# Optimization experiments

Hardware: AMD Instinct MI355X
Metric: run time of the kernel (lower is better)

## Reference

```python
import jax, jax.numpy as jnp
import numpy as np

C = 16            # NCA_channels
LCD = 3           # living_channel_dim
ALPHA = 0.1       # alpha_living_threshold


def _alive(x):
    # F.max_pool3d(x[:, LCD], k=3, s=1, p=1) -> shape [B, D, H, W]
    a = x[:, LCD]
    return jax.lax.reduce_window(a, -jnp.inf, jax.lax.max,
                                 (1, 3, 3, 3), (1, 1, 1, 1), 'SAME')


def _thresh(alive):
    th = ALPHA * jnp.max(alive)
    return jnp.where(jnp.isnan(th), -jnp.inf, th)


def _pw(h, w, b):
    # 1x1x1 Conv3d == per-voxel matmul. h: [B,c,D,H,W], w: [o,c]
    return jnp.einsum('bcdhw,oc->bodhw', h, w) + b[None, :, None, None, None]


def _update(x, w_perc, b_perc, w1, b1, w2, b2, w3, b3):
    alive0 = _alive(x)
    pre_mask = alive0 > _thresh(alive0)
    # depthwise perception conv: C -> 3C, groups=C, k=3, pad=1
    out = jax.lax.conv_general_dilated(
        x, w_perc, (1, 1, 1), 'SAME',
        dimension_numbers=('NCDHW', 'OIDHW', 'NCDHW'),
        feature_group_count=C) + b_perc[None, :, None, None, None]
    # per-voxel MLP: 3C -> h -> h -> C (tanh on hidden layers only)
    out = jnp.tanh(_pw(out, w1, b1))
    out = jnp.tanh(_pw(out, w2, b2))
    out = _pw(out, w3, b3)
    # normalise=False, replace=False -> residual add
    x = x + out
    alive1 = _alive(x)
    post_mask = alive1 > _thresh(alive1)
    life = pre_mask & post_mask          # [B, D, H, W]
    # torch x * life_mask (broadcast valid for B=1)
    return x * life[:, None].astype(x.dtype)


def setup_inputs() -> dict:
    key = jax.random.key(0)
    ks = jax.random.split(key, 10)
    D = 96
    x = jax.random.normal(ks[0], (1, C, D, D, D), dtype=jnp.float32)
    s = 0.1  # keep tanh-NCA dynamics stable
    return {
        'x': x,
        'w_perc': jax.random.normal(ks[1], (3 * C, 1, 3, 3, 3), jnp.float32) * s,
        'b_perc': jax.random.normal(ks[2], (3 * C,), jnp.float32) * s,
        'w1': jax.random.normal(ks[3], (64, 3 * C), jnp.float32) * s,
        'b1': jax.random.normal(ks[4], (64,), jnp.float32) * s,
        'w2': jax.random.normal(ks[5], (64, 64), jnp.float32) * s,
        'b2': jax.random.normal(ks[6], (64,), jnp.float32) * s,
        'w3': jax.random.normal(ks[7], (C, 64), jnp.float32) * s,
        'b3': jax.random.normal(ks[8], (C,), jnp.float32) * s,
        'steps': 4,
        'reading_channel': 4,
        'policy_layers': 2,
        'inOut_out': 48,
    }


def reference(x, w_perc, b_perc, w1, b1, w2, b2, w3, b3,
              steps, reading_channel, policy_layers, inOut_out):
    del reading_channel, policy_layers  # only used for visualization/PCA paths
    for _ in range(steps):
        x = _update(x, w_perc, b_perc, w1, b1, w2, b2, w3, b3)
        # x[:, :, -1, inOutdim[1]:, :] = 0.0
        x = x.at[:, :, -1, inOut_out:, :].set(0.0)
    return x
```

## Files before the change

### kernel.cpp

```cpp
#include <hip/hip_runtime.h>

#define Cn 16
#define Dn 96
#define Sn (Dn*Dn*Dn)
#define DSTRIDE (Dn*Dn)
#define ENC_NEG_INF 0x007FFFFFu
#define PSTR 52

typedef float v2f __attribute__((ext_vector_type(2)));
typedef float v4f __attribute__((ext_vector_type(4)));
typedef _Float16 v4h __attribute__((ext_vector_type(4)));

__device__ __forceinline__ v2f ld2(const float* p){
    v2f r; __builtin_memcpy(&r, p, 8); return r;
}
__device__ __forceinline__ unsigned encf(float f){
    unsigned u = __float_as_uint(f);
    return (u & 0x80000000u) ? ~u : (u | 0x80000000u);
}
__device__ __forceinline__ float decf(unsigned u){
    return (u & 0x80000000u) ? __uint_as_float(u ^ 0x80000000u) : __uint_as_float(~u);
}
__device__ __forceinline__ float ftanh(float x){
    float t = __expf(2.0f*x);
    return 1.0f - __fdividef(2.0f, t + 1.0f);
}
__device__ __forceinline__ int clampi(int v){ return v<0?0:(v>Dn-1?Dn-1:v); }

__global__ void init_kernel(unsigned* __restrict__ maxv){
    if (threadIdx.x < 16) maxv[threadIdx.x] = ENC_NEG_INF;
}

__global__ void tr_kernel(const float* __restrict__ wp, const float* __restrict__ bp,
                          float* __restrict__ wpT, float* __restrict__ bpP){
    const int i = blockIdx.x*256 + threadIdx.x;
    if (i < 1296){ const int t=i/48, r=i%48, q=r>>4, c=r&15; wpT[i] = wp[(3*c+q)*27 + t]; }
    if (i < 48)  { const int q=i>>4, c=i&15; bpP[i] = bp[3*c + q]; }
}

__global__ void pack_kernel(const float* __restrict__ w1, const float* __restrict__ w2,
                            const float* __restrict__ w3,
                            _Float16* __restrict__ w1Ah, _Float16* __restrict__ w1Al,
                            _Float16* __restrict__ w2Ah, _Float16* __restrict__ w2Al,
                            _Float16* __restrict__ w3Ah, _Float16* __restrict__ w3Al){
    const int i = blockIdx.x*256 + threadIdx.x;
    const int e = i & 3, l = (i>>2) & 63, tile = i >> 8;
    const int lr = l & 15, lg = l >> 4;
    if (i < 3072){
        const int ks = tile % 3, mt = tile / 3;
        const int c = 4*lg + e;
        const float v = w1[(16*mt + lr)*48 + 3*c + ks];
        const _Float16 hh = (_Float16)v;
        w1Ah[i] = hh; w1Al[i] = (_Float16)(v - (float)hh);
    }
    if (i < 4096){
        const int ks = tile & 3, mt = tile >> 2;
        const float v = w2[(16*mt + lr)*64 + 16*ks + 4*lg + e];
        const _Float16 hh = (_Float16)v;
        w2Ah[i] = hh; w2Al[i] = (_Float16)(v - (float)hh);
    }
    if (i < 1024){
        const int ks = tile;
        const float v = w3[lr*64 + 16*ks + 4*lg + e];
        const _Float16 hh = (_Float16)v;
        w3Ah[i] = hh; w3Al[i] = (_Float16)(v - (float)hh);
    }
}

__global__ __launch_bounds__(256) void prep_kernel(const float* __restrict__ x3,
    unsigned char* __restrict__ maskA, unsigned* __restrict__ slot)
{
    const int idx = blockIdx.x*256 + threadIdx.x;
    maskA[idx] = 1;
    float v = x3[idx];
    #pragma unroll
    for (int o=32;o;o>>=1) v = fmaxf(v, __shfl_down(v, o));
    __shared__ float red[4];
    const int lane = threadIdx.x & 63, wid = threadIdx.x >> 6;
    if (lane==0) red[wid]=v;
    __syncthreads();
    if (threadIdx.x==0){
        float m = fmaxf(fmaxf(red[0],red[1]), fmaxf(red[2],red[3]));
        atomicMax(slot, encf(m));
    }
}

struct XBuf { float x[16]; float m; int v; };

__device__ __forceinline__ void prefetch_t(int t, int d, int h, int w,
    const float* __restrict__ xin, const unsigned char* __restrict__ min_, XBuf& B)
{
    const int zz = d + t/9 - 1;
    const int yy = h + (t/3)%3 - 1;
    const int xx = w + t%3 - 1;
    const int zc = clampi(zz), yc = clampi(yy), xc = clampi(xx);
    B.v = (zz==zc) & (yy==yc) & (xx==xc);
    const int noff = zc*DSTRIDE + yc*Dn + xc;
    B.m = (float)min_[noff];
    #pragma unroll
    for (int c=0;c<16;++c) B.x[c] = xin[(size_t)c*Sn + noff];
}

__device__ __forceinline__ void accum_t(int t, const XBuf& A,
    const float* __restrict__ wpT, v2f* pv)
{
    const float mv = A.v ? A.m : 0.0f;
    const v2f mvv = {mv, mv};
    const float* wrow = wpT + t*48;
    #pragma unroll
    for (int i=0;i<8;++i){
        v2f xv = {A.x[2*i], A.x[2*i+1]};
        v2f xm = xv * mvv;
        pv[i]    = __builtin_elementwise_fma(ld2(wrow + 2*i),      xm, pv[i]);
        pv[8+i]  = __builtin_elementwise_fma(ld2(wrow + 16 + 2*i), xm, pv[8+i]);
        pv[16+i] = __builtin_elementwise_fma(ld2(wrow + 32 + 2*i), xm, pv[16+i]);
    }
}

__global__ __launch_bounds__(256, 2) void update_kernel(
    const float* __restrict__ xin, const unsigned char* __restrict__ min_,
    float* __restrict__ xout,
    const float* __restrict__ wpT, const float* __restrict__ bpP,
    const _Float16* __restrict__ w1Ah, const _Float16* __restrict__ w1Al,
    const float* __restrict__ b1,
    const _Float16* __restrict__ w2Ah, const _Float16* __restrict__ w2Al,
    const float* __restrict__ b2,
    const _Float16* __restrict__ w3Ah, const _Float16* __restrict__ w3Al,
    const float* __restrict__ b3,
    unsigned* __restrict__ slot_post)
{
    __shared__ __align__(16) float sP[256*PSTR];

    const int tid = threadIdx.x;
    const int w = blockIdx.x*32 + (tid & 31);
    const int h = blockIdx.y*8  + (tid >> 5);
    const int d = blockIdx.z;
    const int idx = d*DSTRIDE + h*Dn + w;

    const int lane = tid & 63;
    const int wv   = tid >> 6;
    const int lr   = lane & 15;
    const int lg   = lane >> 4;

    v2f pv[24];
    #pragma unroll
    for (int j=0;j<24;++j) pv[j] = ld2(bpP + 2*j);

    XBuf A, B;
    prefetch_t(0, d, h, w, xin, min_, A);
    #pragma unroll 1
    for (int t=0; t<26; t+=2){
        prefetch_t(t+1, d, h, w, xin, min_, B);
        accum_t(t, A, wpT, pv);
        prefetch_t(t+2, d, h, w, xin, min_, A);
        accum_t(t+1, B, wpT, pv);
    }
    accum_t(26, A, wpT, pv);

    {
        float* pr = sP + tid*PSTR;
        #pragma unroll
        for (int jj=0;jj<12;++jj){
            v4f t = {pv[2*jj].x, pv[2*jj].y, pv[2*jj+1].x, pv[2*jj+1].y};
            __builtin_memcpy(pr + 4*jj, &t, 16);
        }
    }

    const int rowbase = 64*wv;
    #pragma unroll 1
    for (int half=0; half<2; ++half){
        const int r0 = rowbase + 32*half + lr;
        const int r1 = r0 + 16;

        __builtin_amdgcn_s_setprio(1);
        v4f c1[4][2];
        #pragma unroll
        for (int mt=0;mt<4;++mt){
            v4f bb; __builtin_memcpy(&bb, b1 + 16*mt + 4*lg, 16);
            c1[mt][0]=bb; c1[mt][1]=bb;
        }
        #pragma unroll
        for (int ks=0;ks<3;++ks){
            v4h bh[2], bl[2];
            #pragma unroll
            for (int jj=0;jj<2;++jj){
                v4f P;
                __builtin_memcpy(&P, sP + (jj ? r1 : r0)*PSTR + 16*ks + 4*lg, 16);
                v4h hi = {(_Float16)P[0],(_Float16)P[1],(_Float16)P[2],(_Float16)P[3]};
                v4h lo = {(_Float16)(P[0]-(float)hi[0]), (_Float16)(P[1]-(float)hi[1]),
                          (_Float16)(P[2]-(float)hi[2]), (_Float16)(P[3]-(float)hi[3])};
                bh[jj]=hi; bl[jj]=lo;
            }
            #pragma unroll
            for (int mt=0;mt<4;++mt){
                v4h ah, al;
                __builtin_memcpy(&ah, w1Ah + ((mt*3+ks)*64 + lane)*4, 8);
                __builtin_memcpy(&al, w1Al + ((mt*3+ks)*64 + lane)*4, 8);
                #pragma unroll
                for (int jj=0;jj<2;++jj){
                    c1[mt][jj] = __builtin_amdgcn_mfma_f32_16x16x16f16(ah, bh[jj], c1[mt][jj],0,0,0);
                    c1[mt][jj] = __builtin_amdgcn_mfma_f32_16x16x16f16(al, bh[jj], c1[mt][jj],0,0,0);
                    c1[mt][jj] = __builtin_amdgcn_mfma_f32_16x16x16f16(ah, bl[jj], c1[mt][jj],0,0,0);
                }
            }
        }

        v4f c2[4][2];
        #pragma unroll
        for (int mt=0;mt<4;++mt){
            v4f bb; __builtin_memcpy(&bb, b2 + 16*mt + 4*lg, 16);
            c2[mt][0]=bb; c2[mt][1]=bb;
        }
        #pragma unroll
        for (int ks=0;ks<4;++ks){
            v4h bh[2], bl[2];
            #pragma unroll
            for (int jj=0;jj<2;++jj){
                float t0=ftanh(c1[ks][jj][0]), t1=ftanh(c1[ks][jj][1]);
                float t2=ftanh(c1[ks][jj][2]), t3=ftanh(c1[ks][jj][3]);
                v4h hi = {(_Float16)t0,(_Float16)t1,(_Float16)t2,(_Float16)t3};
                v4h lo = {(_Float16)(t0-(float)hi[0]), (_Float16)(t1-(float)hi[1]),
                          (_Float16)(t2-(float)hi[2]), (_Float16)(t3-(float)hi[3])};
                bh[jj]=hi; bl[jj]=lo;
            }
            #pragma unroll
            for (int mt=0;mt<4;++mt){
                v4h ah, al;
                __builtin_memcpy(&ah, w2Ah + ((mt*4+ks)*64 + lane)*4, 8);
                __builtin_memcpy(&al, w2Al + ((mt*4+ks)*64 + lane)*4, 8);
                #pragma unroll
                for (int jj=0;jj<2;++jj){
                    c2[mt][jj] = __builtin_amdgcn_mfma_f32_16x16x16f16(ah, bh[jj], c2[mt][jj],0,0,0);
                    c2[mt][jj] = __builtin_amdgcn_mfma_f32_16x16x16f16(al, bh[jj], c2[mt][jj],0,0,0);
                    c2[mt][jj] = __builtin_amdgcn_mfma_f32_16x16x16f16(ah, bl[jj], c2[mt][jj],0,0,0);
                }
            }
        }

        v4f c3[2];
        {
            v4f bb; __builtin_memcpy(&bb, b3 + 4*lg, 16);
            c3[0]=bb; c3[1]=bb;
        }
        #pragma unroll
        for (int ks=0;ks<4;++ks){
            v4h bh[2], bl[2];
            #pragma unroll
            for (int jj=0;jj<2;++jj){
                float t0=ftanh(c2[ks][jj][0]), t1=ftanh(c2[ks][jj][1]);
                float t2=ftanh(c2[ks][jj][2]), t3=ftanh(c2[ks][jj][3]);
                v4h hi = {(_Float16)t0,(_Float16)t1,(_Float16)t2,(_Float16)t3};
                v4h lo = {(_Float16)(t0-(float)hi[0]), (_Float16)(t1-(float)hi[1]),
                          (_Float16)(t2-(float)hi[2]), (_Float16)(t3-(float)hi[3])};
                bh[jj]=hi; bl[jj]=lo;
            }
            v4h ah, al;
            __builtin_memcpy(&ah, w3Ah + (ks*64 + lane)*4, 8);
            __builtin_memcpy(&al, w3Al + (ks*64 + lane)*4, 8);
            #pragma unroll
            for (int jj=0;jj<2;++jj){
                c3[jj] = __builtin_amdgcn_mfma_f32_16x16x16f16(ah, bh[jj], c3[jj],0,0,0);
                c3[jj] = __builtin_amdgcn_mfma_f32_16x16x16f16(al, bh[jj], c3[jj],0,0,0);
                c3[jj] = __builtin_amdgcn_mfma_f32_16x16x16f16(ah, bl[jj], c3[jj],0,0,0);
            }
        }
        __builtin_amdgcn_s_setprio(0);

        __builtin_memcpy(sP + r0*PSTR + 4*lg, &c3[0], 16);
        __builtin_memcpy(sP + r1*PSTR + 4*lg, &c3[1], 16);
    }

    const float mcen = (float)min_[idx];
    const float* orow = sP + tid*PSTR;
    float v3 = 0.0f;
    #pragma unroll
    for (int c=0;c<16;++c){
        const float xn = fmaf(xin[(size_t)c*Sn+idx], mcen, orow[c]);
        xout[(size_t)c*Sn+idx] = xn;
        if (c==3) v3 = xn;
    }

    #pragma unroll
    for (int o=32;o;o>>=1) v3 = fmaxf(v3, __shfl_down(v3, o));
    if ((tid & 63) == 0) atomicMax(slot_post, encf(v3));
}

__global__ __launch_bounds__(256) void mask_kernel(
    const float* __restrict__ x3old, const unsigned char* __restrict__ min_,
    const float* __restrict__ x3new, unsigned char* __restrict__ mout,
    const unsigned* __restrict__ slot_pre, const unsigned* __restrict__ slot_post,
    unsigned* __restrict__ slot_next)
{
    const int idx = blockIdx.x*256 + threadIdx.x;
    const int w = idx % Dn;
    const int h = (idx / Dn) % Dn;
    const int d = idx / DSTRIDE;
    const float th0 = 0.1f * decf(*slot_pre);
    const float th1 = 0.1f * decf(*slot_post);
    float a0 = -INFINITY, a1 = -INFINITY;
    #pragma unroll
    for (int t=0;t<27;++t){
        const int dz=t/9-1, dy=(t/3)%3-1, dx=t%3-1;
        const int zz=d+dz, yy=h+dy, xx=w+dx;
        if ((unsigned)zz<(unsigned)Dn && (unsigned)yy<(unsigned)Dn &&
            (unsigned)xx<(unsigned)Dn){
            const int noff = idx + dz*DSTRIDE + dy*Dn + dx;
            a0 = fmaxf(a0, x3old[noff] * (float)min_[noff]);
            a1 = fmaxf(a1, x3new[noff]);
        }
    }
    const bool life = (a0 > th0) && (a1 > th1) && !(d==Dn-1 && h>=48);
    mout[idx] = life ? 1 : 0;
    const float mv = life ? 1.0f : 0.0f;

    float f3 = x3new[idx]*mv;
    #pragma unroll
    for (int o=32;o;o>>=1) f3 = fmaxf(f3, __shfl_down(f3, o));
    __shared__ float red[4];
    const int lane = threadIdx.x & 63, wid = threadIdx.x >> 6;
    if (lane==0) red[wid]=f3;
    __syncthreads();
    if (threadIdx.x==0){
        float m = fmaxf(fmaxf(red[0],red[1]), fmaxf(red[2],red[3]));
        atomicMax(slot_next, encf(m));
    }
}

__global__ __launch_bounds__(256) void apply_kernel(float* __restrict__ x,
    const unsigned char* __restrict__ mk)
{
    const int idx = blockIdx.x*256 + threadIdx.x;
    const float m = (float)mk[idx];
    #pragma unroll
    for (int c=0;c<Cn;++c) x[(size_t)c*Sn+idx] *= m;
}

extern "C" void kernel_launch(void* const* d_in, const int* in_sizes, int n_in,
                              void* d_out, int out_size, void* d_ws, size_t ws_size,
                              hipStream_t stream)
{
    const float* x0 = (const float*)d_in[0];
    const float* wp = (const float*)d_in[1];
    const float* bp = (const float*)d_in[2];
    const float* w1 = (const float*)d_in[3];
    const float* b1 = (const float*)d_in[4];
    const float* w2 = (const float*)d_in[5];
    const float* b2 = (const float*)d_in[6];
    const float* w3 = (const float*)d_in[7];
    const float* b3 = (const float*)d_in[8];
    float* out = (float*)d_out;

    float* T0 = (float*)d_ws;
    unsigned char* mA = (unsigned char*)(T0 + (size_t)Cn*Sn);
    unsigned char* mB = mA + Sn;
    unsigned* maxv = (unsigned*)(mB + Sn);
    float* wpT = (float*)(maxv + 16);
    float* bpP = wpT + 1296;
    _Float16* w1Ah = (_Float16*)(bpP + 48);
    _Float16* w1Al = w1Ah + 3072;
    _Float16* w2Ah = w1Al + 3072;
    _Float16* w2Al = w2Ah + 4096;
    _Float16* w3Ah = w2Al + 4096;
    _Float16* w3Al = w3Ah + 1024;

    init_kernel<<<1, 64, 0, stream>>>(maxv);
    tr_kernel<<<6, 256, 0, stream>>>(wp, bp, wpT, bpP);
    pack_kernel<<<16, 256, 0, stream>>>(w1, w2, w3, w1Ah, w1Al, w2Ah, w2Al, w3Ah, w3Al);
    prep_kernel<<<Sn/256, 256, 0, stream>>>(x0 + (size_t)3*Sn, mA, &maxv[0]);

    const float* xi[4] = {x0, T0, out, T0};
    float*       xo[4] = {T0, out, T0, out};
    const unsigned char* mi[4] = {mA, mB, mA, mB};
    unsigned char*       mo[4] = {mB, mA, mB, mA};

    dim3 ugrid(Dn/32, Dn/8, Dn);
    for (int s=0; s<4; ++s){
        update_kernel<<<ugrid, 256, 0, stream>>>(xi[s], mi[s], xo[s],
            wpT, bpP, w1Ah, w1Al, b1, w2Ah, w2Al, b2, w3Ah, w3Al, b3, &maxv[2*s+1]);
        mask_kernel<<<Sn/256, 256, 0, stream>>>(xi[s] + (size_t)3*Sn, mi[s],
            xo[s] + (size_t)3*Sn, mo[s], &maxv[2*s], &maxv[2*s+1], &maxv[2*s+2]);
    }
    apply_kernel<<<Sn/256, 256, 0, stream>>>(out, mA);
}
```

Before: 1.422 ms.

## Store intermediate state in channel-grouped float4 layout for vectorized neighbor loads

Adds a transpose kernel that rearranges the 16-channel state into four planes of interleaved float4 groups, so each stencil tap in the update kernel does four 16-byte loads instead of sixteen scalar strided loads. Intermediate steps write this layout, and the last step writes the planar output. The living channel is also written to a separate contiguous plane when workspace allows, so the mask kernel can read it without a strided access. This costs an extra transpose pass and extra workspace, and neighbor accesses are now 16-byte strided rather than coalesced per channel.

```diff
diff --git a/kernel.cpp b/kernel.cpp
--- a/kernel.cpp
+++ b/kernel.cpp
@@ -85,10 +85,24 @@
     }
 }
 
-struct XBuf { float x[16]; float m; int v; };
+__global__ __launch_bounds__(256) void transpose_kernel(const float* __restrict__ x,
+    float* __restrict__ xT)
+{
+    const int idx = blockIdx.x*256 + threadIdx.x;
+    float v[16];
+    #pragma unroll
+    for (int c=0;c<16;++c) v[c] = x[(size_t)c*Sn + idx];
+    #pragma unroll
+    for (int g=0;g<4;++g){
+        v4f t = {v[4*g], v[4*g+1], v[4*g+2], v[4*g+3]};
+        __builtin_memcpy(xT + ((size_t)g*Sn + idx)*4, &t, 16);
+    }
+}
+
+struct XBufT { v4f x[4]; float m; int v; };
 
 __device__ __forceinline__ void prefetch_t(int t, int d, int h, int w,
-    const float* __restrict__ xin, const unsigned char* __restrict__ min_, XBuf& B)
+    const float* __restrict__ xt, const unsigned char* __restrict__ min_, XBufT& B)
 {
     const int zz = d + t/9 - 1;
     const int yy = h + (t/3)%3 - 1;
@@ -98,10 +112,11 @@
     const int noff = zc*DSTRIDE + yc*Dn + xc;
     B.m = (float)min_[noff];
     #pragma unroll
-    for (int c=0;c<16;++c) B.x[c] = xin[(size_t)c*Sn + noff];
-}
-
-__device__ __forceinline__ void accum_t(int t, const XBuf& A,
+    for (int g=0;g<4;++g)
+        __builtin_memcpy(&B.x[g], xt + ((size_t)g*Sn + noff)*4, 16);
+}
+
+__device__ __forceinline__ void accum_t(int t, const XBufT& A,
     const float* __restrict__ wpT, v2f* pv)
 {
     const float mv = A.v ? A.m : 0.0f;
@@ -109,7 +124,7 @@
     const float* wrow = wpT + t*48;
     #pragma unroll
     for (int i=0;i<8;++i){
-        v2f xv = {A.x[2*i], A.x[2*i+1]};
+        v2f xv = { A.x[i>>1][2*(i&1)], A.x[i>>1][2*(i&1)+1] };
         v2f xm = xv * mvv;
         pv[i]    = __builtin_elementwise_fma(ld2(wrow + 2*i),      xm, pv[i]);
         pv[8+i]  = __builtin_elementwise_fma(ld2(wrow + 16 + 2*i), xm, pv[8+i]);
@@ -118,8 +133,8 @@
 }
 
 __global__ __launch_bounds__(256, 2) void update_kernel(
-    const float* __restrict__ xin, const unsigned char* __restrict__ min_,
-    float* __restrict__ xout,
+    const float* __restrict__ xinT, const unsigned char* __restrict__ min_,
+    float* __restrict__ xout, const int final_, float* __restrict__ x3out,
     const float* __restrict__ wpT, const float* __restrict__ bpP,
     const _Float16* __restrict__ w1Ah, const _Float16* __restrict__ w1Al,
     const float* __restrict__ b1,
@@ -146,13 +161,13 @@
     #pragma unroll
     for (int j=0;j<24;++j) pv[j] = ld2(bpP + 2*j);
 
-    XBuf A, B;
-    prefetch_t(0, d, h, w, xin, min_, A);
+    XBufT A, B;
+    prefetch_t(0, d, h, w, xinT, min_, A);
     #pragma unroll 1
     for (int t=0; t<26; t+=2){
-        prefetch_t(t+1, d, h, w, xin, min_, B);
+        prefetch_t(t+1, d, h, w, xinT, min_, B);
         accum_t(t, A, wpT, pv);
-        prefetch_t(t+2, d, h, w, xin, min_, A);
+        prefetch_t(t+2, d, h, w, xinT, min_, A);
         accum_t(t+1, B, wpT, pv);
     }
     accum_t(26, A, wpT, pv);
@@ -273,11 +288,28 @@
     const float mcen = (float)min_[idx];
     const float* orow = sP + tid*PSTR;
     float v3 = 0.0f;
-    #pragma unroll
-    for (int c=0;c<16;++c){
-        const float xn = fmaf(xin[(size_t)c*Sn+idx], mcen, orow[c]);
-        xout[(size_t)c*Sn+idx] = xn;
-        if (c==3) v3 = xn;
+    if (!final_){
+        #pragma unroll
+        for (int g=0;g<4;++g){
+            v4f xc; __builtin_memcpy(&xc, xinT + ((size_t)g*Sn + idx)*4, 16);
+            v4f xn;
+            #pragma unroll
+            for (int e=0;e<4;++e) xn[e] = fmaf(xc[e], mcen, orow[4*g+e]);
+            __builtin_memcpy(xout + ((size_t)g*Sn + idx)*4, &xn, 16);
+            if (g==0) v3 = xn[3];
+        }
+        if (x3out) x3out[idx] = v3;
+    } else {
+        #pragma unroll
+        for (int g=0;g<4;++g){
+            v4f xc; __builtin_memcpy(&xc, xinT + ((size_t)g*Sn + idx)*4, 16);
+            #pragma unroll
+            for (int e=0;e<4;++e){
+                const float xn = fmaf(xc[e], mcen, orow[4*g+e]);
+                xout[(size_t)(4*g+e)*Sn + idx] = xn;
+                if (g==0 && e==3) v3 = xn;
+            }
+        }
     }
 
     #pragma unroll
@@ -286,8 +318,10 @@
 }
 
 __global__ __launch_bounds__(256) void mask_kernel(
-    const float* __restrict__ x3old, const unsigned char* __restrict__ min_,
-    const float* __restrict__ x3new, unsigned char* __restrict__ mout,
+    const float* __restrict__ a0src, const int a0_t,
+    const unsigned char* __restrict__ min_,
+    const float* __restrict__ a1src, const int a1_t,
+    unsigned char* __restrict__ mout,
     const unsigned* __restrict__ slot_pre, const unsigned* __restrict__ slot_post,
     unsigned* __restrict__ slot_next)
 {
@@ -305,15 +339,18 @@
         if ((unsigned)zz<(unsigned)Dn && (unsigned)yy<(unsigned)Dn &&
             (unsigned)xx<(unsigned)Dn){
             const int noff = idx + dz*DSTRIDE + dy*Dn + dx;
-            a0 = fmaxf(a0, x3old[noff] * (float)min_[noff]);
-            a1 = fmaxf(a1, x3new[noff]);
+            const float x0v = a0_t ? a0src[(size_t)noff*4+3] : a0src[noff];
+            const float x1v = a1_t ? a1src[(size_t)noff*4+3] : a1src[noff];
+            a0 = fmaxf(a0, x0v * (float)min_[noff]);
+            a1 = fmaxf(a1, x1v);
         }
     }
     const bool life = (a0 > th0) && (a1 > th1) && !(d==Dn-1 && h>=48);
     mout[idx] = life ? 1 : 0;
     const float mv = life ? 1.0f : 0.0f;
 
-    float f3 = x3new[idx]*mv;
+    const float xv3 = a1_t ? a1src[(size_t)idx*4+3] : a1src[idx];
+    float f3 = xv3*mv;
     #pragma unroll
     for (int o=32;o;o>>=1) f3 = fmaxf(f3, __shfl_down(f3, o));
     __shared__ float red[4];
@@ -362,23 +399,41 @@
     _Float16* w2Al = w2Ah + 4096;
     _Float16* w3Ah = w2Al + 4096;
     _Float16* w3Al = w3Ah + 1024;
+    float* Pbase = (float*)(w3Al + 1024);
+    const size_t need = (size_t)((char*)(Pbase + 2*(size_t)Sn) - (char*)d_ws);
+    const bool planes = (ws_size >= need);
+    float* P[2] = { Pbase, Pbase + Sn };
+    float* T1 = out;
 
     init_kernel<<<1, 64, 0, stream>>>(maxv);
     tr_kernel<<<6, 256, 0, stream>>>(wp, bp, wpT, bpP);
     pack_kernel<<<16, 256, 0, stream>>>(w1, w2, w3, w1Ah, w1Al, w2Ah, w2Al, w3Ah, w3Al);
     prep_kernel<<<Sn/256, 256, 0, stream>>>(x0 + (size_t)3*Sn, mA, &maxv[0]);
-
-    const float* xi[4] = {x0, T0, out, T0};
-    float*       xo[4] = {T0, out, T0, out};
+    transpose_kernel<<<Sn/256, 256, 0, stream>>>(x0, T1);
+
+    const float* xiT[4] = {T1, T0, T1, T0};
+    float*       xo[4]  = {T0, T1, T0, out};
+    const int    fin[4] = {0, 0, 0, 1};
     const unsigned char* mi[4] = {mA, mB, mA, mB};
     unsigned char*       mo[4] = {mB, mA, mB, mA};
 
     dim3 ugrid(Dn/32, Dn/8, Dn);
     for (int s=0; s<4; ++s){
-        update_kernel<<<ugrid, 256, 0, stream>>>(xi[s], mi[s], xo[s],
+        float* x3o = (planes && s<3) ? P[s&1] : nullptr;
+        update_kernel<<<ugrid, 256, 0, stream>>>(xiT[s], mi[s], xo[s], fin[s], x3o,
             wpT, bpP, w1Ah, w1Al, b1, w2Ah, w2Al, b2, w3Ah, w3Al, b3, &maxv[2*s+1]);
-        mask_kernel<<<Sn/256, 256, 0, stream>>>(xi[s] + (size_t)3*Sn, mi[s],
-            xo[s] + (size_t)3*Sn, mo[s], &maxv[2*s], &maxv[2*s+1], &maxv[2*s+2]);
+
+        const float* a0src; int a0t;
+        if (s==0){ a0src = x0 + (size_t)3*Sn; a0t = 0; }
+        else if (planes){ a0src = P[(s-1)&1]; a0t = 0; }
+        else { a0src = xiT[s]; a0t = 1; }
+        const float* a1src; int a1t;
+        if (s==3){ a1src = out + (size_t)3*Sn; a1t = 0; }
+        else if (planes){ a1src = P[s&1]; a1t = 0; }
+        else { a1src = xo[s]; a1t = 1; }
+
+        mask_kernel<<<Sn/256, 256, 0, stream>>>(a0src, a0t, mi[s], a1src, a1t,
+            mo[s], &maxv[2*s], &maxv[2*s+1], &maxv[2*s+2]);
     }
     apply_kernel<<<Sn/256, 256, 0, stream>>>(out, mA);
 }
```

Result: faster. 1.325 ms (-6.8%).
